# Optimization experiments

Hardware: AMD Instinct MI355X
Metric: run time of the kernel (lower is better)

Reference implementation:

```python
import jax, jax.numpy as jnp
import numpy as np
import math

H = 8        # num_heads
DK = 64      # key_dim
DV = 64      # value_dim
FACTOR = 4


def setup_inputs() -> dict:
    key = jax.random.key(0)
    B, T, S, D = 4, 2048, 2048, 512
    Dout = H * DV
    ks = jax.random.split(key, 16)
    sample_k = min(int(FACTOR * math.log(S)), S)  # = 33
    inp = {
        "x_q": jax.random.normal(ks[0], (B, T, D), jnp.float32),
        "x_k": jax.random.normal(ks[1], (B, S, D), jnp.float32),
        "x_v": jax.random.normal(ks[2], (B, S, D), jnp.float32),
        "Wq": jax.random.normal(ks[3], (D, H * DK), jnp.float32) * 0.02,
        "bq": jnp.zeros((H * DK,), jnp.float32),
        "Wk": jax.random.normal(ks[4], (D, H * DK), jnp.float32) * 0.02,
        "bk": jnp.zeros((H * DK,), jnp.float32),
        "Wv": jax.random.normal(ks[5], (D, H * DV), jnp.float32) * 0.02,
        "bv": jnp.zeros((H * DV,), jnp.float32),
        "Wo": jax.random.normal(ks[6], (H * DV, Dout), jnp.float32) * 0.02,
        "bo": jnp.zeros((Dout,), jnp.float32),
        "index_sample": jax.random.randint(ks[7], (T, sample_k), 0, S, jnp.int32),
    }
    return inp


def reference(x_q, x_k, x_v, Wq, bq, Wk, bk, Wv, bv, Wo, bo, index_sample):
    B, T, D = x_q.shape
    S = x_k.shape[1]
    u = min(int(FACTOR * math.log(T)), T)  # n_top queries kept

    q = (x_q @ Wq + bq).reshape(B, T, H, DK)
    k = (x_k @ Wk + bk).reshape(B, S, H, DK)
    v = (x_v @ Wv + bv).reshape(B, S, H, DV)

    # --- _prob_QK: sampled QK to score queries ---
    ks = k[:, index_sample]                                  # [B,T,J,H,dk]
    qk_s = jnp.einsum('bthd,btjhd->bthj', q, ks)             # [B,T,H,J]
    M = qk_s.max(-1) - qk_s.mean(-1)                         # [B,T,H]
    _, top = jax.lax.top_k(jnp.transpose(M, (0, 2, 1)), u)   # [B,H,u]

    b_idx = jnp.arange(B)[:, None, None]
    h_idx = jnp.arange(H)[None, :, None]
    q_red = q[b_idx, top, h_idx]                             # [B,H,u,dk]
    qk = jnp.einsum('bhud,bshd->bhus', q_red, k)             # [B,H,u,S]

    # --- s0: default (no mask) context = mean of values over S ---
    ctx = jnp.broadcast_to(v.mean(axis=1, keepdims=True), (B, T, H, DV))
    ctx = jnp.transpose(ctx, (0, 2, 1, 3))                   # [B,H,T,dv]

    # --- s1: scaled softmax over full keys for top queries ---
    scores = jax.nn.softmax(qk * (1.0 / math.sqrt(DK)), axis=-1)
    attn = jnp.einsum('bhus,bshd->bhud', scores, v)          # [B,H,u,dv]

    # --- scatter top-query results into context / scores ---
    ctx = ctx.at[b_idx, h_idx, top].set(attn)                # [B,H,T,dv]
    final_scores = jnp.full((B, H, T, S), 1.0 / S, dtype=scores.dtype)
    final_scores = final_scores.at[b_idx, h_idx, top].set(scores)

    out = jnp.transpose(ctx, (0, 2, 1, 3)).reshape(B, T, H * DV)
    out = out @ Wo + bo                                      # [B,T,output_dim]
    return out, final_scores
```

## Files before the change

kernel.cpp:

```cpp
#include <hip/hip_runtime.h>

typedef __attribute__((ext_vector_type(8))) short short8;
typedef __attribute__((ext_vector_type(4))) float f32x4;

constexpr int Bn  = 4;
constexpr int Tn  = 2048;
constexpr int Sn  = 2048;
constexpr int Dn  = 512;
constexpr int Hn  = 8;
constexpr int DKn = 64;
constexpr int DVn = 64;
constexpr int HDn = 512;
constexpr int SKn = 30;
constexpr int Un  = 30;
constexpr int Gu  = 6;
constexpr int NGroups = Un / Gu;
constexpr int NAttnG  = Bn * Hn * NGroups;
constexpr int NOutF   = (Bn * Tn) / 8;
constexpr int NGemm  = 768;
constexpr float kScale = 0.125f;

constexpr int NWsplit = 192;
constexpr int NVPart  = 64;
constexpr int NSampled = Bn * Tn;
constexpr int NFillS  = (Bn * Hn * Tn) / 4;

__device__ __forceinline__ ushort bf16_rne(float x) {
  unsigned u = __float_as_uint(x);
  return (ushort)((u + 0x7fffu + ((u >> 16) & 1u)) >> 16);
}
__device__ __forceinline__ float bf16f(ushort h) {
  return __uint_as_float(((unsigned)h) << 16);
}
__device__ __forceinline__ void nt_store4(f32x4* p, f32x4 v) {
  __builtin_nontemporal_store(v, p);
}

#define MFMA(accv, av, bv) \
  asm volatile("v_mfma_f32_16x16x32_bf16 %0, %1, %2, %0" : "+v"(accv) : "v"(av), "v"(bv))

__global__ __launch_bounds__(256) void prep_split_kernel(
    const float* __restrict__ Wq, const float* __restrict__ Wk, const float* __restrict__ Wv,
    ushort* __restrict__ WtH, ushort* __restrict__ WtL) {
  const int tid = threadIdx.x;
  const int bid = blockIdx.x;

  const int z = bid / 64, t = bid % 64;
  const int k0 = (t >> 3) * 64, n0 = (t & 7) * 64;
  const float* W = (z == 0) ? Wq : (z == 1) ? Wk : Wv;
  __shared__ float tile[64][65];
  const int r = tid >> 2, c0 = (tid & 3) * 16;
#pragma unroll
  for (int i = 0; i < 16; i += 4) {
    const float4 vv = *(const float4*)(W + (size_t)(k0 + r) * HDn + n0 + c0 + i);
    tile[r][c0 + i] = vv.x; tile[r][c0 + i + 1] = vv.y;
    tile[r][c0 + i + 2] = vv.z; tile[r][c0 + i + 3] = vv.w;
  }
  __syncthreads();
  unsigned hp[8], lp[8];
#pragma unroll
  for (int i = 0; i < 16; i += 2) {
    const float x0 = tile[c0 + i][r];
    const float x1 = tile[c0 + i + 1][r];
    const ushort h0 = bf16_rne(x0), h1 = bf16_rne(x1);
    const ushort l0 = bf16_rne(x0 - bf16f(h0)), l1 = bf16_rne(x1 - bf16f(h1));
    hp[i >> 1] = (unsigned)h0 | ((unsigned)h1 << 16);
    lp[i >> 1] = (unsigned)l0 | ((unsigned)l1 << 16);
  }
  const size_t off = (size_t)(z * 512 + n0 + r) * 512 + k0 + c0;
  *(uint4*)(WtH + off)     = make_uint4(hp[0], hp[1], hp[2], hp[3]);
  *(uint4*)(WtH + off + 8) = make_uint4(hp[4], hp[5], hp[6], hp[7]);
  *(uint4*)(WtL + off)     = make_uint4(lp[0], lp[1], lp[2], lp[3]);
  *(uint4*)(WtL + off + 8) = make_uint4(lp[4], lp[5], lp[6], lp[7]);
}

__global__ __launch_bounds__(256, 2) void gemm_kernel(
    const float* __restrict__ xq, const float* __restrict__ xk, const float* __restrict__ xv,
    const ushort* __restrict__ WtH, const ushort* __restrict__ WtL,
    const float* __restrict__ bq, const float* __restrict__ bk, const float* __restrict__ bv,
    float* __restrict__ qo, float* __restrict__ ko, float* __restrict__ vo) {
  const int bid = blockIdx.x;
  const int tid = threadIdx.x;

  __shared__ ushort AsH[64][32];
  __shared__ ushort AsL[64][32];
  __shared__ ushort BsH[256][32];
  __shared__ ushort BsL[256][32];

  const int z = bid >> 8;
  const int rem = bid & 255;
  const int bm = (rem >> 1) * 64;
  const int bn = (rem & 1) * 256;
  const float* X = (z == 0) ? xq : (z == 1) ? xk : xv;
  const float* bias = (z == 0) ? bq : (z == 1) ? bk : bv;
  float* Y = (z == 0) ? qo : (z == 1) ? ko : vo;

  const int lane = tid & 63;
  const int wave = tid >> 6;
  const int fr = lane & 15;
  const int gk = lane >> 4;

  const int ar = tid >> 2, ag = tid & 3;
  const float* xrow = X + (size_t)(bm + ar) * Dn + ag * 8;
  const int brow0 = tid >> 2, bg = tid & 3;
  const ushort* wh = WtH + (size_t)(z * 512 + bn + brow0) * 512 + bg * 8;
  const ushort* wl = WtL + (size_t)(z * 512 + bn + brow0) * 512 + bg * 8;

  f32x4 acc[4][4];
#pragma unroll
  for (int m = 0; m < 4; ++m)
#pragma unroll
    for (int n = 0; n < 4; ++n)
#pragma unroll
      for (int j = 0; j < 4; ++j) acc[m][n][j] = 0.f;

  float4 af0, af1;
  uint4 sbH[4], sbL[4];
#define STG_LOAD(k0_) do { \
    af0 = *(const float4*)(xrow + (k0_)); \
    af1 = *(const float4*)(xrow + (k0_) + 4); \
    sbH[0] = *(const uint4*)(wh + (k0_));          sbL[0] = *(const uint4*)(wl + (k0_)); \
    sbH[1] = *(const uint4*)(wh + (k0_) + 32768);  sbL[1] = *(const uint4*)(wl + (k0_) + 32768); \
    sbH[2] = *(const uint4*)(wh + (k0_) + 65536);  sbL[2] = *(const uint4*)(wl + (k0_) + 65536); \
    sbH[3] = *(const uint4*)(wh + (k0_) + 98304);  sbL[3] = *(const uint4*)(wl + (k0_) + 98304); \
  } while (0)

  const int agq = (ag ^ ((ar >> 1) & 3)) * 8;
  const int bgx = bg ^ ((brow0 >> 1) & 3);
  const int gq = (gk ^ ((fr >> 1) & 3)) * 8;

  STG_LOAD(0);
  for (int k0 = 0; k0 < Dn; k0 += 32) {
    __syncthreads();
    {
      float xf[8] = {af0.x, af0.y, af0.z, af0.w, af1.x, af1.y, af1.z, af1.w};
      unsigned hp[4], lp[4];
#pragma unroll
      for (int i = 0; i < 8; i += 2) {
        const ushort h0 = bf16_rne(xf[i]), h1 = bf16_rne(xf[i + 1]);
        const ushort l0 = bf16_rne(xf[i] - bf16f(h0)), l1 = bf16_rne(xf[i + 1] - bf16f(h1));
        hp[i >> 1] = (unsigned)h0 | ((unsigned)h1 << 16);
        lp[i >> 1] = (unsigned)l0 | ((unsigned)l1 << 16);
      }
      *(uint4*)&AsH[ar][agq] = make_uint4(hp[0], hp[1], hp[2], hp[3]);
      *(uint4*)&AsL[ar][agq] = make_uint4(lp[0], lp[1], lp[2], lp[3]);
#pragma unroll
      for (int p = 0; p < 4; ++p) {
        const int n = brow0 + p * 64;
        *(uint4*)&BsH[n][bgx * 8] = sbH[p];
        *(uint4*)&BsL[n][bgx * 8] = sbL[p];
      }
    }
    __syncthreads();
    if (k0 + 32 < Dn) STG_LOAD(k0 + 32);

    short8 aH[4], aL[4], bH[4], bL[4];
#pragma unroll
    for (int m = 0; m < 4; ++m) {
      aH[m] = *(const short8*)&AsH[m * 16 + fr][gq];
      aL[m] = *(const short8*)&AsL[m * 16 + fr][gq];
    }
#pragma unroll
    for (int n = 0; n < 4; ++n) {
      bH[n] = *(const short8*)&BsH[wave * 64 + n * 16 + fr][gq];
      bL[n] = *(const short8*)&BsL[wave * 64 + n * 16 + fr][gq];
    }
#pragma unroll
    for (int m = 0; m < 4; ++m)
#pragma unroll
      for (int n = 0; n < 4; ++n) {
        MFMA(acc[m][n], aH[m], bH[n]);
        MFMA(acc[m][n], aH[m], bL[n]);
        MFMA(acc[m][n], aL[m], bH[n]);
      }
  }
  asm volatile("s_nop 7\n\ts_nop 7");

  float bsv[4];
#pragma unroll
  for (int n = 0; n < 4; ++n) bsv[n] = bias[bn + wave * 64 + n * 16 + fr];
#pragma unroll
  for (int m = 0; m < 4; ++m) {
#pragma unroll
    for (int n = 0; n < 4; ++n) {
      const int col = bn + wave * 64 + n * 16 + fr;
#pragma unroll
      for (int j = 0; j < 4; ++j) {
        Y[(size_t)(bm + m * 16 + gk * 4 + j) * HDn + col] = acc[m][n][j] + bsv[n];
      }
    }
  }
#undef STG_LOAD
}

__global__ __launch_bounds__(64) void sampled_m_kernel(
    const float* __restrict__ q, const float* __restrict__ k,
    const int* __restrict__ idxs, float* __restrict__ Mt,
    const float* __restrict__ v, float* __restrict__ vpart,
    float* __restrict__ fscores) {
  const int bid = blockIdx.x;
  const int lane = threadIdx.x;

  if (bid >= NVPart + NSampled) {
    const size_t fb = (size_t)(bid - NVPart - NSampled);
    const float c = 1.0f / Sn;
    const f32x4 c4v = {c, c, c, c};
    f32x4* p = (f32x4*)fscores + fb * 2048;
#pragma unroll
    for (int i = 0; i < 32; ++i) nt_store4(p + i * 64 + lane, c4v);
    return;
  }

  if (bid < NVPart) {
    const int pb = bid;
    const int b = pb >> 4, part = pb & 15;
    const float4* v4 = (const float4*)(v + (size_t)b * Sn * HDn);
    float4 a0 = make_float4(0.f, 0.f, 0.f, 0.f);
    float4 a1 = make_float4(0.f, 0.f, 0.f, 0.f);
    const int s0 = part * 128;
    for (int s = s0; s < s0 + 128; ++s) {
      const float4 x0 = v4[(size_t)s * 128 + lane * 2];
      const float4 x1 = v4[(size_t)s * 128 + lane * 2 + 1];
      a0.x += x0.x; a0.y += x0.y; a0.z += x0.z; a0.w += x0.w;
      a1.x += x1.x; a1.y += x1.y; a1.z += x1.z; a1.w += x1.w;
    }
    float4* vp4 = (float4*)vpart + (size_t)pb * 128;
    vp4[lane * 2] = a0; vp4[lane * 2 + 1] = a1;
    return;
  }

  const int inner = bid - NVPart;
  const int x = inner & 7;
  const int b = x & 3;
  const int t = ((inner >> 3) << 1) | (x >> 2);

  const int sg = lane >> 3;
  const int d8 = lane & 7;
  __shared__ int sidx[32];
  if (lane < SKn) sidx[lane] = idxs[t * SKn + lane];
  if (lane >= SKn && lane < 32) sidx[lane] = 0;
  __syncthreads();
  const float* qrow = q + ((size_t)(b * Tn + t)) * HDn;
  const float* kb = k + (size_t)b * Sn * HDn;
  for (int h = 0; h < Hn; ++h) {
    const float4 qv0 = *(const float4*)(qrow + h * DKn + d8 * 8);
    const float4 qv1 = *(const float4*)(qrow + h * DKn + d8 * 8 + 4);
    float mx = -1e30f, sum = 0.f;
#pragma unroll
    for (int jb = 0; jb < 32; jb += 8) {
      const int j = jb + sg;
      const int srow = sidx[j];
      const float* kr = kb + (size_t)srow * HDn + h * DKn + d8 * 8;
      const float4 kv0 = *(const float4*)kr;
      const float4 kv1 = *(const float4*)(kr + 4);
      float p = kv0.x * qv0.x + kv0.y * qv0.y + kv0.z * qv0.z + kv0.w * qv0.w
              + kv1.x * qv1.x + kv1.y * qv1.y + kv1.z * qv1.z + kv1.w * qv1.w;
      p += __shfl_xor(p, 1);
      p += __shfl_xor(p, 2);
      p += __shfl_xor(p, 4);
      if (j < SKn) { mx = fmaxf(mx, p); sum += p; }
    }
    mx = fmaxf(mx, __shfl_xor(mx, 8));
    mx = fmaxf(mx, __shfl_xor(mx, 16));
    mx = fmaxf(mx, __shfl_xor(mx, 32));
    sum += __shfl_xor(sum, 8);
    sum += __shfl_xor(sum, 16);
    sum += __shfl_xor(sum, 32);
    if (lane == 0) Mt[((size_t)(b * Hn + h)) * Tn + t] = mx - sum * (1.0f / SKn);
  }
}

__global__ __launch_bounds__(256) void topk_vmean_base_kernel(
    const float* __restrict__ Mt, const float* __restrict__ vpart,
    const float* __restrict__ Wo, const float* __restrict__ bo,
    int* __restrict__ top, float* __restrict__ vmean, float* __restrict__ basep) {
  const int tid = threadIdx.x;
  const int lane = tid & 63, w = tid >> 6;
  __shared__ float vals[Tn];
  __shared__ float wv[4];
  __shared__ int wi[4];
  __shared__ float4 part[256];
  __shared__ float vm[HDn];

  if (blockIdx.x < 32) {
    const int bh = blockIdx.x;
    for (int i = tid; i < Tn; i += 256) vals[i] = Mt[(size_t)bh * Tn + i];
    __syncthreads();
    for (int u = 0; u < Un; ++u) {
      float bv = -1e30f; int bi = 0x7fffffff;
      for (int i = tid; i < Tn; i += 256) {
        const float x = vals[i];
        if (x > bv) { bv = x; bi = i; }
      }
#pragma unroll
      for (int o = 1; o < 64; o <<= 1) {
        const float ov = __shfl_xor(bv, o);
        const int oi = __shfl_xor(bi, o);
        if (ov > bv || (ov == bv && oi < bi)) { bv = ov; bi = oi; }
      }
      if (lane == 0) { wv[w] = bv; wi[w] = bi; }
      __syncthreads();
      bv = wv[0]; bi = wi[0];
#pragma unroll
      for (int j = 1; j < 4; ++j) {
        if (wv[j] > bv || (wv[j] == bv && wi[j] < bi)) { bv = wv[j]; bi = wi[j]; }
      }
      if (tid == 0) { top[bh * Un + u] = bi; vals[bi] = -1e30f; }
      __syncthreads();
    }
  } else {
    const int b = blockIdx.x - 32;
    const int c4 = tid & 127, half = tid >> 7;
    float4 acc = make_float4(0.f, 0.f, 0.f, 0.f);
    for (int p = half * 8; p < half * 8 + 8; ++p) {
      const float4 x = ((const float4*)vpart)[(size_t)(b * 16 + p) * 128 + c4];
      acc.x += x.x; acc.y += x.y; acc.z += x.z; acc.w += x.w;
    }
    part[tid] = acc;
    __syncthreads();
    if (half == 0) {
      float4 a = part[c4], bpp = part[128 + c4];
      const float sc = 1.0f / Sn;
      float4 r = make_float4((a.x + bpp.x) * sc, (a.y + bpp.y) * sc,
                             (a.z + bpp.z) * sc, (a.w + bpp.w) * sc);
      *(float4*)(vm + c4 * 4) = r;
      *(float4*)(vmean + b * HDn + c4 * 4) = r;
    }
    __syncthreads();
    const float4* Wo4 = (const float4*)Wo;
    float4 acc2 = make_float4(0.f, 0.f, 0.f, 0.f);
    for (int c = half * 256; c < half * 256 + 256; ++c) {
      const float vmc = vm[c];
      const float4 wrow = Wo4[(size_t)c * 128 + c4];
      acc2.x += vmc * wrow.x; acc2.y += vmc * wrow.y;
      acc2.z += vmc * wrow.z; acc2.w += vmc * wrow.w;
    }
    __syncthreads();
    part[tid] = acc2;
    __syncthreads();
    if (half == 0) {
      float4 a = part[c4], bpp = part[128 + c4];
      const float4 bb = ((const float4*)bo)[c4];
      float4 r = make_float4(a.x + bpp.x + bb.x, a.y + bpp.y + bb.y,
                             a.z + bpp.z + bb.z, a.w + bpp.w + bb.w);
      ((float4*)basep)[b * 128 + c4] = r;
    }
  }
}

__global__ __launch_bounds__(256) void attn_out_kernel(
    const float* __restrict__ q, const float* __restrict__ k,
    const float* __restrict__ v, const float* __restrict__ vmean,
    const int* __restrict__ top, const float* __restrict__ Wo,
    const float* __restrict__ basep,
    float* __restrict__ out, float* __restrict__ fscores) {
  const int tid = threadIdx.x;
  const int bid = blockIdx.x;

  if (bid >= NAttnG) {
    const int fid = bid - NAttnG;
    const int r0 = fid * 8;
    const int b = r0 >> 11;
    const int t0 = r0 & (Tn - 1);
    __shared__ int sflag8[8];
    if (tid < 8) sflag8[tid] = 0;
    __syncthreads();
    if (tid < Hn * Un) {
      const int d = top[b * Hn * Un + tid] - t0;
      if (d >= 0 && d < 8) sflag8[d] = 1;
    }
    __syncthreads();
    const int col4 = tid & 127, rh = tid >> 7;
    const float4 bv4 = ((const float4*)basep)[b * 128 + col4];
    const f32x4 bvx = {bv4.x, bv4.y, bv4.z, bv4.w};
#pragma unroll
    for (int rp = 0; rp < 4; ++rp) {
      const int rr = rp * 2 + rh;
      float4* orow4 = (float4*)(out + (size_t)(r0 + rr) * HDn) + col4;
      if (sflag8[rr]) {
        float* p = (float*)orow4;
        atomicAdd(p + 0, bv4.x); atomicAdd(p + 1, bv4.y);
        atomicAdd(p + 2, bv4.z); atomicAdd(p + 3, bv4.w);
      } else {
        nt_store4((f32x4*)orow4, bvx);
      }
    }
    return;
  }

  const int xs = bid & 7;
  const int b = xs & 3;
  const int combo = (bid >> 3) + (xs >> 2) * 20;
  const int h = combo / 5;
  const int grp = combo % 5;
  const int bh = b * Hn + h;
  const int u0 = grp * Gu;
  const int lane = tid & 63, w = tid >> 6;

  __shared__ float qs[Gu][DKn];
  __shared__ float sc[Gu][2052];
  __shared__ float red[8];
  __shared__ int tsel[Gu];
  __shared__ float4 partv[4][Gu][16];

  if (tid < Gu) tsel[tid] = top[bh * Un + u0 + tid];
  __syncthreads();
  for (int i = tid; i < Gu * DKn; i += 256) {
    const int g = i >> 6, d = i & 63;
    qs[g][d] = q[((size_t)(b * Tn + tsel[g])) * HDn + h * DKn + d];
  }
  __syncthreads();

  const float4* k4 = (const float4*)k;
  for (int s = tid; s < Sn; s += 256) {
    const float4* krow = k4 + ((size_t)(b * Sn + s)) * 128 + h * 16;
    float acc[Gu];
#pragma unroll
    for (int g = 0; g < Gu; ++g) acc[g] = 0.f;
#pragma unroll
    for (int d4i = 0; d4i < 16; ++d4i) {
      const float4 kv = krow[d4i];
#pragma unroll
      for (int g = 0; g < Gu; ++g) {
        const float4 qv = *(const float4*)&qs[g][d4i * 4];
        acc[g] += kv.x * qv.x + kv.y * qv.y + kv.z * qv.z + kv.w * qv.w;
      }
    }
#pragma unroll
    for (int g = 0; g < Gu; ++g) sc[g][s] = acc[g] * kScale;
  }
  __syncthreads();

  float invs[Gu];
#pragma unroll
  for (int g = 0; g < Gu; ++g) {
    float lm = -1e30f;
    for (int i = tid; i < Sn; i += 256) lm = fmaxf(lm, sc[g][i]);
#pragma unroll
    for (int o = 1; o < 64; o <<= 1) lm = fmaxf(lm, __shfl_xor(lm, o));
    if (lane == 0) red[w] = lm;
    __syncthreads();
    const float mx = fmaxf(fmaxf(red[0], red[1]), fmaxf(red[2], red[3]));
    float ls = 0.f;
    for (int i = tid; i < Sn; i += 256) {
      const float e = __expf(sc[g][i] - mx);
      sc[g][i] = e;
      ls += e;
    }
#pragma unroll
    for (int o = 1; o < 64; o <<= 1) ls += __shfl_xor(ls, o);
    if (lane == 0) red[4 + w] = ls;
    __syncthreads();
    invs[g] = 1.0f / (red[4] + red[5] + red[6] + red[7]);
    __syncthreads();
  }
#pragma unroll
  for (int g = 0; g < Gu; ++g) {
    const float inv = invs[g];
    float4* scg4 = (float4*)sc[g];
    f32x4* fsrow4 = (f32x4*)(fscores + ((size_t)bh * Tn + tsel[g]) * Sn);
#pragma unroll
    for (int it = 0; it < 2; ++it) {
      const int i = it * 256 + tid;
      float4 p = scg4[i];
      p.x *= inv; p.y *= inv; p.z *= inv; p.w *= inv;
      scg4[i] = p;
      const f32x4 px = {p.x, p.y, p.z, p.w};
      nt_store4(fsrow4 + i, px);
    }
  }
  __syncthreads();

  const int d4 = lane & 15;
  const int sg = (w << 2) + (lane >> 4);
  const float4* v4 = (const float4*)v;
  float4 pacc[Gu];
#pragma unroll
  for (int g = 0; g < Gu; ++g) pacc[g] = make_float4(0.f, 0.f, 0.f, 0.f);
  for (int s = sg; s < Sn; s += 16) {
    const float4 vv = v4[((size_t)(b * Sn + s)) * 128 + h * 16 + d4];
#pragma unroll
    for (int g = 0; g < Gu; ++g) {
      const float p = sc[g][s];
      pacc[g].x += p * vv.x; pacc[g].y += p * vv.y;
      pacc[g].z += p * vv.z; pacc[g].w += p * vv.w;
    }
  }
#pragma unroll
  for (int g = 0; g < Gu; ++g) {
#pragma unroll
    for (int o = 16; o < 64; o <<= 1) {
      pacc[g].x += __shfl_xor(pacc[g].x, o);
      pacc[g].y += __shfl_xor(pacc[g].y, o);
      pacc[g].z += __shfl_xor(pacc[g].z, o);
      pacc[g].w += __shfl_xor(pacc[g].w, o);
    }
    if (lane < 16) partv[w][g][lane] = pacc[g];
  }
  __syncthreads();
  if (tid < Gu * 16) {
    const int g = tid >> 4, dd = tid & 15;
    float4 r = partv[0][g][dd];
    const float4 r1 = partv[1][g][dd], r2 = partv[2][g][dd], r3 = partv[3][g][dd];
    r.x += r1.x + r2.x + r3.x; r.y += r1.y + r2.y + r3.y;
    r.z += r1.z + r2.z + r3.z; r.w += r1.w + r2.w + r3.w;
    const float4 vm4 = ((const float4*)vmean)[bh * 16 + dd];
    r.x -= vm4.x; r.y -= vm4.y; r.z -= vm4.z; r.w -= vm4.w;
    *(float4*)&qs[g][dd * 4] = r;
  }
  __syncthreads();

  const int col4 = tid & 127, gg = tid >> 7;
  const float4* Wo4 = (const float4*)Wo;
#pragma unroll
  for (int gp = 0; gp < Gu / 2; ++gp) {
    const int g = gp * 2 + gg;
    float4 a = make_float4(0.f, 0.f, 0.f, 0.f);
#pragma unroll
    for (int d = 0; d < DKn; ++d) {
      const float dv = qs[g][d];
      const float4 wrow = Wo4[(size_t)(h * DKn + d) * 128 + col4];
      a.x += dv * wrow.x; a.y += dv * wrow.y;
      a.z += dv * wrow.z; a.w += dv * wrow.w;
    }
    float* orow = out + ((size_t)(b * Tn + tsel[g])) * HDn + col4 * 4;
    atomicAdd(orow + 0, a.x); atomicAdd(orow + 1, a.y);
    atomicAdd(orow + 2, a.z); atomicAdd(orow + 3, a.w);
  }
}

extern "C" void kernel_launch(void* const* d_in, const int* in_sizes, int n_in,
                              void* d_out, int out_size, void* d_ws, size_t ws_size,
                              hipStream_t stream) {
  const float* x_q = (const float*)d_in[0];
  const float* x_k = (const float*)d_in[1];
  const float* x_v = (const float*)d_in[2];
  const float* Wq = (const float*)d_in[3];
  const float* bq = (const float*)d_in[4];
  const float* Wk = (const float*)d_in[5];
  const float* bk = (const float*)d_in[6];
  const float* Wv = (const float*)d_in[7];
  const float* bv = (const float*)d_in[8];
  const float* Wo = (const float*)d_in[9];
  const float* bo = (const float*)d_in[10];
  const int* idx = (const int*)d_in[11];

  float* out = (float*)d_out;
  float* fscores = out + (size_t)Bn * Tn * HDn;

  float* ws = (float*)d_ws;
  float* q = ws;
  float* kp = ws + (size_t)4194304;
  float* vp = ws + (size_t)8388608;
  float* Mt = ws + (size_t)12582912;
  float* vmean = ws + (size_t)12648448;
  float* basep = ws + (size_t)12650496;
  int* top = (int*)(ws + (size_t)12652544);
  float* vpart = ws + (size_t)12656640;

  char* scr = (char*)(fscores + (size_t)49152 * Sn);
  ushort* WtH = (ushort*)scr;
  ushort* WtL = WtH + (size_t)3 * 512 * 512;

  prep_split_kernel<<<NWsplit, 256, 0, stream>>>(Wq, Wk, Wv, WtH, WtL);

  gemm_kernel<<<NGemm, 256, 0, stream>>>(
      x_q, x_k, x_v, WtH, WtL, bq, bk, bv, q, kp, vp);

  sampled_m_kernel<<<NVPart + NSampled + NFillS, 64, 0, stream>>>(
      q, kp, idx, Mt, vp, vpart, fscores);

  topk_vmean_base_kernel<<<36, 256, 0, stream>>>(Mt, vpart, Wo, bo, top, vmean, basep);

  attn_out_kernel<<<NAttnG + NOutF, 256, 0, stream>>>(
      q, kp, vp, vmean, top, Wo, basep, out, fscores);
}
```

Measured before the change: 910.5 us.

## Spread constant score fill across gemm, sampled, and topk kernels

The 1/S fill of the large final_scores tensor was previously done entirely inside the sampled-M kernel. It is now split three ways: one share goes to extra blocks in the GEMM kernel, one stays in the sampled kernel, and one goes to extra blocks in the top-k kernel. The aim is to overlap this bandwidth-heavy fill with compute-bound or latency-bound phases, especially the near-serial 36-block top-k kernel. The sampled kernel's (b,t) block mapping is also simplified to linear order, which changes the L2 locality of K row accesses.

```diff
diff --git a/kernel.cpp b/kernel.cpp
--- a/kernel.cpp
+++ b/kernel.cpp
@@ -23,7 +23,13 @@
 constexpr int NWsplit = 192;
 constexpr int NVPart  = 64;
 constexpr int NSampled = Bn * Tn;
-constexpr int NFillS  = (Bn * Hn * Tn) / 4;
+
+constexpr int NFillG = 9216;
+constexpr int NFillS = 4608;
+constexpr int NFillT = 2560;
+constexpr int FillRowsG = 0;
+constexpr int FillRowsS = NFillG * 4;
+constexpr int FillRowsT = (NFillG + NFillS) * 4;
 
 __device__ __forceinline__ ushort bf16_rne(float x) {
   unsigned u = __float_as_uint(x);
@@ -34,6 +40,13 @@
 }
 __device__ __forceinline__ void nt_store4(f32x4* p, f32x4 v) {
   __builtin_nontemporal_store(v, p);
+}
+__device__ __forceinline__ void fill_rows4_256(float* fscores, size_t r0, int tid) {
+  const float c = 1.0f / Sn;
+  const f32x4 c4v = {c, c, c, c};
+  f32x4* fs4 = (f32x4*)fscores + r0 * (Sn / 4);
+#pragma unroll
+  for (int i = 0; i < 8; ++i) nt_store4(fs4 + i * 256 + tid, c4v);
 }
 
 #define MFMA(accv, av, bv) \
@@ -74,13 +87,19 @@
   *(uint4*)(WtL + off + 8) = make_uint4(lp[4], lp[5], lp[6], lp[7]);
 }
 
-__global__ __launch_bounds__(256, 2) void gemm_kernel(
+__global__ __launch_bounds__(256, 2) void gemm_fill_kernel(
     const float* __restrict__ xq, const float* __restrict__ xk, const float* __restrict__ xv,
     const ushort* __restrict__ WtH, const ushort* __restrict__ WtL,
     const float* __restrict__ bq, const float* __restrict__ bk, const float* __restrict__ bv,
-    float* __restrict__ qo, float* __restrict__ ko, float* __restrict__ vo) {
+    float* __restrict__ qo, float* __restrict__ ko, float* __restrict__ vo,
+    float* __restrict__ fscores) {
   const int bid = blockIdx.x;
   const int tid = threadIdx.x;
+
+  if (bid >= NGemm) {
+    fill_rows4_256(fscores, (size_t)FillRowsG + (size_t)(bid - NGemm) * 4, tid);
+    return;
+  }
 
   __shared__ ushort AsH[64][32];
   __shared__ ushort AsL[64][32];
@@ -202,10 +221,10 @@
   const int lane = threadIdx.x;
 
   if (bid >= NVPart + NSampled) {
-    const size_t fb = (size_t)(bid - NVPart - NSampled);
+    const size_t r0 = (size_t)FillRowsS + (size_t)(bid - NVPart - NSampled) * 4;
     const float c = 1.0f / Sn;
     const f32x4 c4v = {c, c, c, c};
-    f32x4* p = (f32x4*)fscores + fb * 2048;
+    f32x4* p = (f32x4*)fscores + r0 * (Sn / 4);
 #pragma unroll
     for (int i = 0; i < 32; ++i) nt_store4(p + i * 64 + lane, c4v);
     return;
@@ -230,9 +249,7 @@
   }
 
   const int inner = bid - NVPart;
-  const int x = inner & 7;
-  const int b = x & 3;
-  const int t = ((inner >> 3) << 1) | (x >> 2);
+  const int b = inner >> 11, t = inner & (Tn - 1);
 
   const int sg = lane >> 3;
   const int d8 = lane & 7;
@@ -273,9 +290,16 @@
 __global__ __launch_bounds__(256) void topk_vmean_base_kernel(
     const float* __restrict__ Mt, const float* __restrict__ vpart,
     const float* __restrict__ Wo, const float* __restrict__ bo,
-    int* __restrict__ top, float* __restrict__ vmean, float* __restrict__ basep) {
+    int* __restrict__ top, float* __restrict__ vmean, float* __restrict__ basep,
+    float* __restrict__ fscores) {
   const int tid = threadIdx.x;
   const int lane = tid & 63, w = tid >> 6;
+
+  if (blockIdx.x >= 36) {
+    fill_rows4_256(fscores, (size_t)FillRowsT + (size_t)(blockIdx.x - 36) * 4, tid);
+    return;
+  }
+
   __shared__ float vals[Tn];
   __shared__ float wv[4];
   __shared__ int wi[4];
@@ -564,13 +588,14 @@
 
   prep_split_kernel<<<NWsplit, 256, 0, stream>>>(Wq, Wk, Wv, WtH, WtL);
 
-  gemm_kernel<<<NGemm, 256, 0, stream>>>(
-      x_q, x_k, x_v, WtH, WtL, bq, bk, bv, q, kp, vp);
+  gemm_fill_kernel<<<NGemm + NFillG, 256, 0, stream>>>(
+      x_q, x_k, x_v, WtH, WtL, bq, bk, bv, q, kp, vp, fscores);
 
   sampled_m_kernel<<<NVPart + NSampled + NFillS, 64, 0, stream>>>(
       q, kp, idx, Mt, vp, vpart, fscores);
 
-  topk_vmean_base_kernel<<<36, 256, 0, stream>>>(Mt, vpart, Wo, bo, top, vmean, basep);
+  topk_vmean_base_kernel<<<36 + NFillT, 256, 0, stream>>>(
+      Mt, vpart, Wo, bo, top, vmean, basep, fscores);
 
   attn_out_kernel<<<NAttnG + NOutF, 256, 0, stream>>>(
       q, kp, vp, vmean, top, Wo, basep, out, fscores);
```

Result: no change. 894.3 us (-1.8%).
